# Kernel tuning notes

Measured on AMD Instinct MI355X. Metric: run time of the kernel, lower is better.

The kernel has to match this reference:

```python
import jax, jax.numpy as jnp
import numpy as np

N_EMBD = 1024
N_HEAD = 16
BLOCK_SIZE = 2048
NEG_INF = -1e10


def _rope_cache(head_dim, max_positions):
    # theta_i = 10000^{-2i/dim}, freqs[t, i] = t * theta_i
    theta = 1.0 / (10000.0 ** (jnp.arange(0, head_dim, 2, dtype=jnp.float32) / head_dim))
    freqs = jnp.arange(max_positions, dtype=jnp.float32)[:, None] * theta[None, :]
    return jnp.cos(freqs), jnp.sin(freqs)  # each (max_positions, head_dim//2)


def _apply_rope(x, cos, sin):
    # x: (B, nh, T, hs) interpreted as interleaved complex pairs
    B, nh, T, hs = x.shape
    xr = x.reshape(B, nh, T, hs // 2, 2)
    x0, x1 = xr[..., 0], xr[..., 1]
    c = cos[:T][None, None, :, :]
    s = sin[:T][None, None, :, :]
    o0 = x0 * c - x1 * s
    o1 = x0 * s + x1 * c
    return jnp.stack([o0, o1], axis=-1).reshape(B, nh, T, hs)


def setup_inputs() -> dict:
    key = jax.random.key(0)
    ks = jax.random.split(key, 9)
    B, T, C = 2, 2048, N_EMBD
    sc = 1.0 / np.sqrt(C)
    return {
        "x": jax.random.normal(ks[0], (B, T, C), jnp.float32),
        "Wq": jax.random.normal(ks[1], (C, C), jnp.float32) * sc,
        "bq": jax.random.normal(ks[2], (C,), jnp.float32) * 0.02,
        "Wk": jax.random.normal(ks[3], (C, C), jnp.float32) * sc,
        "bk": jax.random.normal(ks[4], (C,), jnp.float32) * 0.02,
        "Wv": jax.random.normal(ks[5], (C, C), jnp.float32) * sc,
        "bv": jax.random.normal(ks[6], (C,), jnp.float32) * 0.02,
        "Wp": jax.random.normal(ks[7], (C, C), jnp.float32) * sc,
        "bp": jax.random.normal(ks[8], (C,), jnp.float32) * 0.02,
    }


def reference(x, Wq, bq, Wk, bk, Wv, bv, Wp, bp):
    B, T, C = x.shape
    nh, hs = N_HEAD, C // N_HEAD

    def heads(W, b):
        return (x @ W.T + b).reshape(B, T, nh, hs).transpose(0, 2, 1, 3)

    q = heads(Wq, bq)
    k = heads(Wk, bk)
    v = heads(Wv, bv)

    cos, sin = _rope_cache(hs, BLOCK_SIZE)
    q = _apply_rope(q, cos, sin)
    k = _apply_rope(k, cos, sin)

    att = jnp.einsum("bhqd,bhkd->bhqk", q, k) * (1.0 / np.sqrt(hs))
    causal = jnp.tril(jnp.ones((T, T), dtype=bool))
    att = jnp.where(causal[None, None], att, NEG_INF)
    att = jax.nn.softmax(att, axis=-1)
    y = jnp.einsum("bhqk,bhkd->bhqd", att, v)
    y = y.transpose(0, 2, 1, 3).reshape(B, T, C)
    return y @ Wp.T + bp
```

## Files before the change

### kernel.cpp

```cpp
#include <hip/hip_runtime.h>

typedef __bf16 bf16;
typedef short  s16;
typedef s16   s16x8 __attribute__((ext_vector_type(8)));
typedef bf16  bf16x4 __attribute__((ext_vector_type(4)));
typedef float f32x4 __attribute__((ext_vector_type(4)));

#define B_SZ 2
#define T_SEQ 2048
#define C_DIM 1024
#define NH 16
#define HS 64
#define M_TOT (B_SZ * T_SEQ)

#define NEG_BIG (-30000.0f)
#define LOG2_10000 13.287712379549449f
#define Q_PRESCALE 0.18033688011112042f


__device__ __forceinline__ float san(float x) {
    unsigned u = __float_as_uint(x);
    return ((u & 0x7F800000u) == 0x7F800000u) ? 0.f : x;
}

__device__ __forceinline__ void load16_lds(const bf16* g, void* lds_base) {
    __builtin_amdgcn_global_load_lds(
        (const __attribute__((address_space(1))) void*)g,
        (__attribute__((address_space(3))) void*)lds_base, 16, 0, 0);
}

#define CVT_GRID 8448

__global__ __launch_bounds__(256) void cvt_bf16_kernel(
    const float* __restrict__ x,  const float* __restrict__ wq,
    const float* __restrict__ wk, const float* __restrict__ wv,
    const float* __restrict__ wp,
    bf16* __restrict__ xb, bf16* __restrict__ wqb, bf16* __restrict__ wkb,
    bf16* __restrict__ wvb, bf16* __restrict__ wpb,
    float* __restrict__ cs, float* __restrict__ sn)
{
    const int b = blockIdx.x;
    if (b >= 8192) {
        const int idx = (b - 8192) * 256 + threadIdx.x;
        const int t = idx >> 5, i = idx & 31;
        const float theta = __builtin_exp2f(-(float)(2 * i) * (LOG2_10000 / 64.f));
        const float a = (float)t * theta;
        cs[idx] = san(cosf(a));
        sn[idx] = san(sinf(a));
        return;
    }
    int z, base;
    if (b < 4096) { z = 0; base = b; }
    else          { z = 1 + ((b - 4096) >> 10); base = (b - 4096) & 1023; }

    const float* src = (z == 0) ? x : (z == 1) ? wq : (z == 2) ? wk : (z == 3) ? wv : wp;
    bf16* dst = (z == 0) ? xb : (z == 1) ? wqb : (z == 2) ? wkb : (z == 3) ? wvb : wpb;

    const int i = (base * 256 + threadIdx.x) * 4;
    const float4 v = *(const float4*)(src + i);
    bf16x4 o;
    o[0] = (bf16)v.x; o[1] = (bf16)v.y; o[2] = (bf16)v.z; o[3] = (bf16)v.w;
    *(bf16x4*)(dst + i) = o;
}

#define QSTAGE(bufi, kk)                                                       \
    load16_lds(gA + (kk),               (char*)(sA[bufi]) + w * 1024);         \
    load16_lds(gA + 128 * C_DIM + (kk), (char*)(sA[bufi]) + 8192 + w * 1024);  \
    load16_lds(gB + (kk),               (char*)(sB[bufi]) + w * 1024);         \
    load16_lds(gB + 128 * C_DIM + (kk), (char*)(sB[bufi]) + 8192 + w * 1024);

__global__ __launch_bounds__(512, 2) void qkv_gemm(
    const bf16* __restrict__ X, const bf16* __restrict__ W_all,
    const float* __restrict__ bq, const float* __restrict__ bk,
    const float* __restrict__ bv,
    const float* __restrict__ cs_tab, const float* __restrict__ sn_tab,
    bf16* __restrict__ q_ws, bf16* __restrict__ k_ws, bf16* __restrict__ vt_ws)
{
    __shared__ __attribute__((aligned(16))) bf16 sA[3][256 * 32];
    __shared__ __attribute__((aligned(16))) bf16 sB[3][256 * 32];

    const int m0 = blockIdx.x * 256;
    const int n0 = blockIdx.y * 256;
    const int mode = blockIdx.y >> 2;

    const int t = threadIdx.x;
    const int w = t >> 6;
    const int lane = t & 63;
    const int qd = lane >> 4;
    const int r  = lane & 15;
    const int qs = qd ^ ((r >> 1) & 3);
    const int wm = w >> 2, wn = w & 3;
    const int srow = t >> 2;
    const int scol = ((t & 3) ^ ((t >> 3) & 3)) * 8;
    const bf16* gA = X + (size_t)(m0 + srow) * C_DIM + scol;
    const bf16* gB = W_all + (size_t)(n0 + srow) * C_DIM + scol;

    f32x4 acc[8][4] = {};

    QSTAGE(0, 0)
    QSTAGE(1, 32)
    #pragma unroll
    for (int kt_ = 0; kt_ < 32; kt_++) {
        __builtin_amdgcn_sched_barrier(0);
        if (kt_ < 30) asm volatile("s_waitcnt vmcnt(4) lgkmcnt(0)" ::: "memory");
        else          asm volatile("s_waitcnt vmcnt(0) lgkmcnt(0)" ::: "memory");
        __builtin_amdgcn_sched_barrier(0);
        __builtin_amdgcn_s_barrier();
        __builtin_amdgcn_sched_barrier(0);
        if (kt_ + 2 < 32) { QSTAGE((kt_ + 2) % 3, (kt_ + 2) * 32) }
        {
            const bf16* pA = sA[kt_ % 3];
            const bf16* pB = sB[kt_ % 3];
            s16x8 af[8], bfr[4];
            #pragma unroll
            for (int mt = 0; mt < 8; mt++)
                af[mt] = *(const s16x8*)(pA + (wm * 128 + mt * 16 + r) * 32 + qs * 8);
            #pragma unroll
            for (int nt = 0; nt < 4; nt++)
                bfr[nt] = *(const s16x8*)(pB + (wn * 64 + nt * 16 + r) * 32 + qs * 8);
            #pragma unroll
            for (int mt = 0; mt < 8; mt++)
                #pragma unroll
                for (int nt = 0; nt < 4; nt++)
                    acc[mt][nt] = __builtin_amdgcn_mfma_f32_16x16x32_bf16(
                        af[mt], bfr[nt], acc[mt][nt], 0, 0, 0);
        }
    }

    const float* bias = (mode == 0) ? bq : (mode == 1) ? bk : bv;

    if (mode == 2) {
        #pragma unroll
        for (int mt = 0; mt < 8; mt++) {
            const int mrow0 = m0 + wm * 128 + mt * 16 + qd * 4;
            const int bb = mrow0 >> 11;
            const int t0 = mrow0 & 2047;
            #pragma unroll
            for (int nt = 0; nt < 4; nt++) {
                const int cm = (n0 & 1023) + wn * 64 + nt * 16 + r;
                const int h = cm >> 6, d = cm & 63;
                const float bv_ = bias[cm];
                bf16x4 pk;
                #pragma unroll
                for (int reg = 0; reg < 4; reg++)
                    pk[reg] = (bf16)san(acc[mt][nt][reg] + bv_);
                *(bf16x4*)(vt_ws + ((size_t)(bb * NH + h) * HS + d) * T_SEQ + t0) = pk;
            }
        }
    } else {
        bf16* out = (mode == 0) ? q_ws : k_ws;
        const float post = (mode == 0) ? Q_PRESCALE : 1.0f;
        #pragma unroll
        for (int mt = 0; mt < 8; mt++) {
            const int mrow0 = m0 + wm * 128 + mt * 16 + qd * 4;
            const int bb = mrow0 >> 11;
            const int t0 = mrow0 & 2047;
            #pragma unroll
            for (int nt = 0; nt < 4; nt++) {
                const int cm = (n0 & 1023) + wn * 64 + nt * 16 + r;
                const int h = cm >> 6, d = cm & 63;
                const int pi = d >> 1;
                const float bv_ = bias[cm];
                #pragma unroll
                for (int reg = 0; reg < 4; reg++) {
                    const int tt = t0 + reg;
                    float v = san(acc[mt][nt][reg] + bv_);
                    float partner = __shfl_xor(v, 1);
                    float c = cs_tab[tt * 32 + pi];
                    float s = sn_tab[tt * 32 + pi];
                    float rot = (d & 1) ? (v * c + partner * s)
                                        : (v * c - partner * s);
                    out[((size_t)(bb * NH + h) * T_SEQ + tt) * HS + d] =
                        (bf16)san(rot * post);
                }
            }
        }
    }
}

#define STAGE3(bufi, kk)                                                       \
    load16_lds(gA0 + (kk), (char*)(sA + (bufi) * 2048) + w * 1024);            \
    load16_lds(gB0 + (kk), (char*)(sB + (bufi) * 4096) + w * 1024);            \
    load16_lds(gB1 + (kk), (char*)(sB + (bufi) * 4096) + 4096 + w * 1024);

#define K_STEP3(bufi)                                                          \
    {                                                                          \
        const bf16* pA = sA + (bufi) * 2048;                                   \
        const bf16* pB = sB + (bufi) * 4096;                                   \
        s16x8 af[2], bfr[4];                                                   \
        _Pragma("unroll")                                                      \
        for (int mt = 0; mt < 2; mt++)                                         \
            af[mt] = *(const s16x8*)(pA + (wm * 32 + mt * 16 + r) * 32 + qs * 8); \
        _Pragma("unroll")                                                      \
        for (int nt = 0; nt < 4; nt++)                                         \
            bfr[nt] = *(const s16x8*)(pB + (wn * 64 + nt * 16 + r) * 32 + qs * 8); \
        _Pragma("unroll")                                                      \
        for (int mt = 0; mt < 2; mt++)                                         \
            _Pragma("unroll")                                                  \
            for (int nt = 0; nt < 4; nt++)                                     \
                acc[mt][nt] = __builtin_amdgcn_mfma_f32_16x16x32_bf16(         \
                    af[mt], bfr[nt], acc[mt][nt], 0, 0, 0);                    \
    }

#define GEMM_CORE(Xp, Wp_)                                                     \
    const int t = threadIdx.x;                                                 \
    const int w = t >> 6;                                                      \
    const int lane = t & 63;                                                   \
    const int qd = lane >> 4;                                                  \
    const int r  = lane & 15;                                                  \
    const int qs = qd ^ ((r >> 1) & 3);                                        \
    const int wm = w & 1, wn = w >> 1;                                         \
    const int srow = t >> 2;                                                   \
    const int scol = ((t & 3) ^ ((t >> 3) & 3)) * 8;                           \
    const bf16* gA0 = (Xp) + (size_t)(m0 + srow) * C_DIM + scol;               \
    const bf16* gB0 = (Wp_) + (size_t)(n0 + srow) * C_DIM + scol;              \
    const bf16* gB1 = (Wp_) + (size_t)(n0 + 64 + srow) * C_DIM + scol;         \
    f32x4 acc[2][4] = {};                                                      \
    STAGE3(0, 0)                                                               \
    STAGE3(1, 32)                                                              \
    _Pragma("unroll")                                                          \
    for (int kt_ = 0; kt_ < 32; kt_++) {                                       \
        __builtin_amdgcn_sched_barrier(0);                                     \
        if (kt_ < 30) asm volatile("s_waitcnt vmcnt(3) lgkmcnt(0)" ::: "memory"); \
        else          asm volatile("s_waitcnt vmcnt(0) lgkmcnt(0)" ::: "memory"); \
        __builtin_amdgcn_sched_barrier(0);                                     \
        __builtin_amdgcn_s_barrier();                                          \
        __builtin_amdgcn_sched_barrier(0);                                     \
        if (kt_ + 2 < 32) { STAGE3((kt_ + 2) % 3, (kt_ + 2) * 32) }            \
        K_STEP3(kt_ % 3)                                                       \
    }

__global__ __launch_bounds__(256) void proj_gemm(
    const bf16* __restrict__ Y, const bf16* __restrict__ Wp,
    const float* __restrict__ bp, float* __restrict__ out)
{
    __shared__ __attribute__((aligned(16))) bf16 sA[3 * 64 * 32];
    __shared__ __attribute__((aligned(16))) bf16 sB[3 * 128 * 32];

    const int m0 = blockIdx.x * 64;
    const int n0 = blockIdx.y * 128;

    GEMM_CORE(Y, Wp)

    #pragma unroll
    for (int mt = 0; mt < 2; mt++) {
        const int mrow0 = m0 + wm * 32 + mt * 16 + qd * 4;
        #pragma unroll
        for (int nt = 0; nt < 4; nt++) {
            const int col = n0 + wn * 64 + nt * 16 + r;
            const float bv_ = bp[col];
            #pragma unroll
            for (int reg = 0; reg < 4; reg++)
                out[(size_t)(mrow0 + reg) * C_DIM + col] = san(acc[mt][nt][reg] + bv_);
        }
    }
}

__global__ __launch_bounds__(256) void attn_kernel(
    const bf16* __restrict__ q_ws, const bf16* __restrict__ k_ws,
    const bf16* __restrict__ vt_ws, bf16* __restrict__ y_ws)
{
    __shared__ __attribute__((aligned(16))) bf16 sK[2][2][64][32];
    __shared__ __attribute__((aligned(16))) bf16 sV[2][2][64][32];
    __shared__ __attribute__((aligned(16))) bf16 sP[4][16][72];

    const int id = (int)blockIdx.x;
    const int qt = 31 - (id >> 5);
    const int j  = id & 31;
    const int bh = (j & 7) + 8 * (j >> 3);

    const int w    = threadIdx.x >> 6;
    const int lane = threadIdx.x & 63;
    const int qd = lane >> 4;
    const int r  = lane & 15;
    const int qs = qd ^ ((r >> 1) & 3);
    const int ps = 4 * (r & 3);

    const bf16* Qb = q_ws + (size_t)bh * T_SEQ * HS;
    const bf16* Kb = k_ws + (size_t)bh * T_SEQ * HS;
    const bf16* Vb = vt_ws + (size_t)bh * HS * T_SEQ;

    const int srow = lane >> 2;
    const int scol = ((lane & 3) ^ ((lane >> 3) & 3)) * 8;
    const bf16* Kb_w = Kb + (size_t)(w * 16 + srow) * HS + scol;
    const bf16* Vb_w = Vb + (size_t)(w * 16 + srow) * T_SEQ + scol;

    bf16 (*pw)[72] = sP[w];
    const int bb = bh >> 4, h = bh & 15;

    const int q0 = qt * 64 + w * 16;

    s16x8 aq0 = *(const s16x8*)(Qb + (size_t)(q0 + r) * HS + qd * 8);
    s16x8 aq1 = *(const s16x8*)(Qb + (size_t)(q0 + r) * HS + 32 + qd * 8);

    f32x4 o[4] = {};
    float l_lane = 0.f;

    load16_lds(Kb_w,      &sK[0][0][w * 16][0]);
    load16_lds(Kb_w + 32, &sK[0][1][w * 16][0]);
    load16_lds(Vb_w,      &sV[0][0][w * 16][0]);
    load16_lds(Vb_w + 32, &sV[0][1][w * 16][0]);

    for (int kt = 0; kt <= qt; kt++) {
        const int cur = kt & 1;
        __syncthreads();

        if (kt < qt) {
            const bf16* kp = Kb_w + (size_t)(kt + 1) * 64 * HS;
            const bf16* vp = Vb_w + (kt + 1) * 64;
            load16_lds(kp,      &sK[cur ^ 1][0][w * 16][0]);
            load16_lds(kp + 32, &sK[cur ^ 1][1][w * 16][0]);
            load16_lds(vp,      &sV[cur ^ 1][0][w * 16][0]);
            load16_lds(vp + 32, &sV[cur ^ 1][1][w * 16][0]);
        }

        f32x4 s[4];
        __builtin_amdgcn_s_setprio(1);
        #pragma unroll
        for (int c = 0; c < 4; c++) {
            s16x8 k0 = *(const s16x8*)&sK[cur][0][c * 16 + r][qs * 8];
            s16x8 k1 = *(const s16x8*)&sK[cur][1][c * 16 + r][qs * 8];
            f32x4 z = {};
            z = __builtin_amdgcn_mfma_f32_16x16x32_bf16(k0, aq0, z, 0, 0, 0);
            z = __builtin_amdgcn_mfma_f32_16x16x32_bf16(k1, aq1, z, 0, 0, 0);
            s[c] = z;
        }
        __builtin_amdgcn_s_setprio(0);

        if (kt == qt) {
            const int qg = q0 + r;
            #pragma unroll
            for (int c = 0; c < 4; c++)
                #pragma unroll
                for (int reg = 0; reg < 4; reg++) {
                    const int kg = kt * 64 + c * 16 + qd * 4 + reg;
                    s[c][reg] = (kg <= qg) ? s[c][reg] : NEG_BIG;
                }
        }

        #pragma unroll
        for (int c = 0; c < 4; c++) {
            bf16x4 pk;
            #pragma unroll
            for (int reg = 0; reg < 4; reg++) {
                float p = __builtin_exp2f(s[c][reg]);
                l_lane += p;
                pk[reg] = (bf16)p;
            }
            *(bf16x4*)&pw[r][((4 * c + qd) ^ ps) * 4] = pk;
        }

        s16x8 ap0 = *(const s16x8*)&pw[r][((2 * qd) ^ ps) * 4];
        s16x8 ap1 = *(const s16x8*)&pw[r][((8 + 2 * qd) ^ ps) * 4];
        __builtin_amdgcn_s_setprio(1);
        #pragma unroll
        for (int nt = 0; nt < 4; nt++) {
            s16x8 av0 = *(const s16x8*)&sV[cur][0][nt * 16 + r][qs * 8];
            s16x8 av1 = *(const s16x8*)&sV[cur][1][nt * 16 + r][qs * 8];
            o[nt] = __builtin_amdgcn_mfma_f32_16x16x32_bf16(av0, ap0, o[nt], 0, 0, 0);
            o[nt] = __builtin_amdgcn_mfma_f32_16x16x32_bf16(av1, ap1, o[nt], 0, 0, 0);
        }
        __builtin_amdgcn_s_setprio(0);
    }

    float l = l_lane;
    l += __shfl_xor(l, 16);
    l += __shfl_xor(l, 32);
    const float inv = 1.f / fmaxf(l, 1e-20f);

    const int q = q0 + r;
    bf16* dst = y_ws + ((size_t)(bb * T_SEQ + q) * NH + h) * HS;
    #pragma unroll
    for (int nt = 0; nt < 4; nt++) {
        bf16x4 pk;
        #pragma unroll
        for (int reg = 0; reg < 4; reg++)
            pk[reg] = (bf16)san(o[nt][reg] * inv);
        *(bf16x4*)(dst + nt * 16 + qd * 4) = pk;
    }
}

extern "C" void kernel_launch(void* const* d_in, const int* in_sizes, int n_in,
                              void* d_out, int out_size, void* d_ws, size_t ws_size,
                              hipStream_t stream)
{
    const size_t MB = 1024 * 1024;
    const size_t NEED = 40 * MB + 2 * 65536 * sizeof(float);
    if (ws_size < NEED || n_in < 9) return;

    const float* x  = (const float*)d_in[0];
    const float* Wq = (const float*)d_in[1];
    const float* bq = (const float*)d_in[2];
    const float* Wk = (const float*)d_in[3];
    const float* bk = (const float*)d_in[4];
    const float* Wv = (const float*)d_in[5];
    const float* bv = (const float*)d_in[6];
    const float* Wp = (const float*)d_in[7];
    const float* bp = (const float*)d_in[8];
    float* out = (float*)d_out;

    char* ws = (char*)d_ws;
    bf16*  q_ws   = (bf16*)(ws + 0 * MB);
    bf16*  k_ws   = (bf16*)(ws + 8 * MB);
    bf16*  vt_ws  = (bf16*)(ws + 16 * MB);
    bf16*  x_b    = (bf16*)(ws + 24 * MB);
    bf16*  y_ws   = (bf16*)(ws + 24 * MB);
    bf16*  Wq_b   = (bf16*)(ws + 32 * MB);
    bf16*  Wk_b   = (bf16*)(ws + 34 * MB);
    bf16*  Wv_b   = (bf16*)(ws + 36 * MB);
    bf16*  Wp_b   = (bf16*)(ws + 38 * MB);
    float* cs_tab = (float*)(ws + 40 * MB);
    float* sn_tab = cs_tab + 65536;
    const bf16* W_all = Wq_b;

    cvt_bf16_kernel<<<dim3(CVT_GRID), 256, 0, stream>>>(
        x, Wq, Wk, Wv, Wp, x_b, Wq_b, Wk_b, Wv_b, Wp_b, cs_tab, sn_tab);
    qkv_gemm<<<dim3(M_TOT / 256, 3 * C_DIM / 256), 512, 0, stream>>>(
        x_b, W_all, bq, bk, bv, cs_tab, sn_tab, q_ws, k_ws, vt_ws);
    attn_kernel<<<dim3(32 * 32), 256, 0, stream>>>(
        q_ws, k_ws, vt_ws, y_ws);
    proj_gemm<<<dim3(M_TOT / 64, C_DIM / 128), 256, 0, stream>>>(
        y_ws, Wp_b, bp, out);
}
```

Baseline: 184.1 us.

## Process two adjacent query tiles per attention block to share K/V loads

Each attention workgroup now handles a pair of consecutive 64-row query tiles (qtB and qtA = qtB+1) for the same head, so every K/V tile loaded into LDS and the K fragments read from it are reused by both tiles. The grid halves to 512 blocks, and the last diagonal K tile is handled in a separate epilogue for the upper tile only. This cuts K/V global and LDS traffic per query row and evens out causal work per block. In exchange it uses more registers for the doubled Q, score and accumulator state, which may lower occupancy, and leaves fewer blocks to fill the GPU.

After: 215.7 us. 17.2% more time.

```diff
diff --git a/kernel.cpp b/kernel.cpp
--- a/kernel.cpp
+++ b/kernel.cpp
@@ -256,18 +256,50 @@
     }
 }
 
+
+#define ATT_QK(sv, aq0_, aq1_)                                                 \
+    _Pragma("unroll")                                                          \
+    for (int c = 0; c < 4; c++) {                                              \
+        f32x4 z = {};                                                          \
+        z = __builtin_amdgcn_mfma_f32_16x16x32_bf16(kf0[c], aq0_, z, 0, 0, 0); \
+        z = __builtin_amdgcn_mfma_f32_16x16x32_bf16(kf1[c], aq1_, z, 0, 0, 0); \
+        sv[c] = z;                                                             \
+    }
+
+#define ATT_MASK(sv, qg)                                                       \
+    _Pragma("unroll")                                                          \
+    for (int c = 0; c < 4; c++)                                                \
+        _Pragma("unroll")                                                      \
+        for (int reg = 0; reg < 4; reg++) {                                    \
+            const int kg = kt * 64 + c * 16 + qd * 4 + reg;                    \
+            sv[c][reg] = (kg <= (qg)) ? sv[c][reg] : NEG_BIG;                  \
+        }
+
+#define ATT_SM(sv, pbuf, lacc)                                                 \
+    _Pragma("unroll")                                                          \
+    for (int c = 0; c < 4; c++) {                                              \
+        bf16x4 pk;                                                             \
+        _Pragma("unroll")                                                      \
+        for (int reg = 0; reg < 4; reg++) {                                    \
+            float p = __builtin_exp2f(sv[c][reg]);                             \
+            lacc += p;                                                         \
+            pk[reg] = (bf16)p;                                                 \
+        }                                                                      \
+        *(bf16x4*)&pbuf[r][((4 * c + qd) ^ ps) * 4] = pk;                      \
+    }
+
 __global__ __launch_bounds__(256) void attn_kernel(
     const bf16* __restrict__ q_ws, const bf16* __restrict__ k_ws,
     const bf16* __restrict__ vt_ws, bf16* __restrict__ y_ws)
 {
     __shared__ __attribute__((aligned(16))) bf16 sK[2][2][64][32];
     __shared__ __attribute__((aligned(16))) bf16 sV[2][2][64][32];
-    __shared__ __attribute__((aligned(16))) bf16 sP[4][16][72];
+    __shared__ __attribute__((aligned(16))) bf16 sP[2][4][16][72];
 
     const int id = (int)blockIdx.x;
-    const int qt = 31 - (id >> 5);
-    const int j  = id & 31;
-    const int bh = (j & 7) + 8 * (j >> 3);
+    const int bh = (id & 7) + 8 * (id >> 7);
+    const int pr = 15 - ((id >> 3) & 15);
+    const int qtB = 2 * pr, qtA = qtB + 1;
 
     const int w    = threadIdx.x >> 6;
     const int lane = threadIdx.x & 63;
@@ -285,27 +317,31 @@
     const bf16* Kb_w = Kb + (size_t)(w * 16 + srow) * HS + scol;
     const bf16* Vb_w = Vb + (size_t)(w * 16 + srow) * T_SEQ + scol;
 
-    bf16 (*pw)[72] = sP[w];
+    bf16 (*pwA)[72] = sP[0][w];
+    bf16 (*pwB)[72] = sP[1][w];
     const int bb = bh >> 4, h = bh & 15;
 
-    const int q0 = qt * 64 + w * 16;
-
-    s16x8 aq0 = *(const s16x8*)(Qb + (size_t)(q0 + r) * HS + qd * 8);
-    s16x8 aq1 = *(const s16x8*)(Qb + (size_t)(q0 + r) * HS + 32 + qd * 8);
-
-    f32x4 o[4] = {};
-    float l_lane = 0.f;
+    const int q0A = qtA * 64 + w * 16;
+    const int q0B = qtB * 64 + w * 16;
+
+    s16x8 aqA0 = *(const s16x8*)(Qb + (size_t)(q0A + r) * HS + qd * 8);
+    s16x8 aqA1 = *(const s16x8*)(Qb + (size_t)(q0A + r) * HS + 32 + qd * 8);
+    s16x8 aqB0 = *(const s16x8*)(Qb + (size_t)(q0B + r) * HS + qd * 8);
+    s16x8 aqB1 = *(const s16x8*)(Qb + (size_t)(q0B + r) * HS + 32 + qd * 8);
+
+    f32x4 oA[4] = {}, oB[4] = {};
+    float lA = 0.f, lB = 0.f;
 
     load16_lds(Kb_w,      &sK[0][0][w * 16][0]);
     load16_lds(Kb_w + 32, &sK[0][1][w * 16][0]);
     load16_lds(Vb_w,      &sV[0][0][w * 16][0]);
     load16_lds(Vb_w + 32, &sV[0][1][w * 16][0]);
 
-    for (int kt = 0; kt <= qt; kt++) {
+    for (int kt = 0; kt <= qtB; kt++) {
         const int cur = kt & 1;
         __syncthreads();
 
-        if (kt < qt) {
+        {
             const bf16* kp = Kb_w + (size_t)(kt + 1) * 64 * HS;
             const bf16* vp = Vb_w + (kt + 1) * 64;
             load16_lds(kp,      &sK[cur ^ 1][0][w * 16][0]);
@@ -314,69 +350,100 @@
             load16_lds(vp + 32, &sV[cur ^ 1][1][w * 16][0]);
         }
 
-        f32x4 s[4];
+        s16x8 kf0[4], kf1[4];
+        #pragma unroll
+        for (int c = 0; c < 4; c++) {
+            kf0[c] = *(const s16x8*)&sK[cur][0][c * 16 + r][qs * 8];
+            kf1[c] = *(const s16x8*)&sK[cur][1][c * 16 + r][qs * 8];
+        }
+        f32x4 sa[4], sb[4];
         __builtin_amdgcn_s_setprio(1);
-        #pragma unroll
-        for (int c = 0; c < 4; c++) {
-            s16x8 k0 = *(const s16x8*)&sK[cur][0][c * 16 + r][qs * 8];
-            s16x8 k1 = *(const s16x8*)&sK[cur][1][c * 16 + r][qs * 8];
-            f32x4 z = {};
-            z = __builtin_amdgcn_mfma_f32_16x16x32_bf16(k0, aq0, z, 0, 0, 0);
-            z = __builtin_amdgcn_mfma_f32_16x16x32_bf16(k1, aq1, z, 0, 0, 0);
-            s[c] = z;
-        }
+        ATT_QK(sa, aqA0, aqA1)
+        ATT_QK(sb, aqB0, aqB1)
         __builtin_amdgcn_s_setprio(0);
 
-        if (kt == qt) {
-            const int qg = q0 + r;
-            #pragma unroll
-            for (int c = 0; c < 4; c++)
-                #pragma unroll
-                for (int reg = 0; reg < 4; reg++) {
-                    const int kg = kt * 64 + c * 16 + qd * 4 + reg;
-                    s[c][reg] = (kg <= qg) ? s[c][reg] : NEG_BIG;
-                }
-        }
-
-        #pragma unroll
-        for (int c = 0; c < 4; c++) {
-            bf16x4 pk;
-            #pragma unroll
-            for (int reg = 0; reg < 4; reg++) {
-                float p = __builtin_exp2f(s[c][reg]);
-                l_lane += p;
-                pk[reg] = (bf16)p;
-            }
-            *(bf16x4*)&pw[r][((4 * c + qd) ^ ps) * 4] = pk;
-        }
-
-        s16x8 ap0 = *(const s16x8*)&pw[r][((2 * qd) ^ ps) * 4];
-        s16x8 ap1 = *(const s16x8*)&pw[r][((8 + 2 * qd) ^ ps) * 4];
+        if (kt == qtB) { ATT_MASK(sb, q0B + r) }
+
+        ATT_SM(sa, pwA, lA)
+        ATT_SM(sb, pwB, lB)
+
+        s16x8 apA0 = *(const s16x8*)&pwA[r][((2 * qd) ^ ps) * 4];
+        s16x8 apA1 = *(const s16x8*)&pwA[r][((8 + 2 * qd) ^ ps) * 4];
+        s16x8 apB0 = *(const s16x8*)&pwB[r][((2 * qd) ^ ps) * 4];
+        s16x8 apB1 = *(const s16x8*)&pwB[r][((8 + 2 * qd) ^ ps) * 4];
         __builtin_amdgcn_s_setprio(1);
         #pragma unroll
         for (int nt = 0; nt < 4; nt++) {
             s16x8 av0 = *(const s16x8*)&sV[cur][0][nt * 16 + r][qs * 8];
             s16x8 av1 = *(const s16x8*)&sV[cur][1][nt * 16 + r][qs * 8];
-            o[nt] = __builtin_amdgcn_mfma_f32_16x16x32_bf16(av0, ap0, o[nt], 0, 0, 0);
-            o[nt] = __builtin_amdgcn_mfma_f32_16x16x32_bf16(av1, ap1, o[nt], 0, 0, 0);
+            oA[nt] = __builtin_amdgcn_mfma_f32_16x16x32_bf16(av0, apA0, oA[nt], 0, 0, 0);
+            oA[nt] = __builtin_amdgcn_mfma_f32_16x16x32_bf16(av1, apA1, oA[nt], 0, 0, 0);
+            oB[nt] = __builtin_amdgcn_mfma_f32_16x16x32_bf16(av0, apB0, oB[nt], 0, 0, 0);
+            oB[nt] = __builtin_amdgcn_mfma_f32_16x16x32_bf16(av1, apB1, oB[nt], 0, 0, 0);
         }
         __builtin_amdgcn_s_setprio(0);
     }
 
-    float l = l_lane;
-    l += __shfl_xor(l, 16);
-    l += __shfl_xor(l, 32);
-    const float inv = 1.f / fmaxf(l, 1e-20f);
-
-    const int q = q0 + r;
-    bf16* dst = y_ws + ((size_t)(bb * T_SEQ + q) * NH + h) * HS;
-    #pragma unroll
-    for (int nt = 0; nt < 4; nt++) {
-        bf16x4 pk;
-        #pragma unroll
-        for (int reg = 0; reg < 4; reg++)
-            pk[reg] = (bf16)san(o[nt][reg] * inv);
-        *(bf16x4*)(dst + nt * 16 + qd * 4) = pk;
+    {
+        const int kt = qtA;
+        const int cur = kt & 1;
+        __syncthreads();
+
+        s16x8 kf0[4], kf1[4];
+        #pragma unroll
+        for (int c = 0; c < 4; c++) {
+            kf0[c] = *(const s16x8*)&sK[cur][0][c * 16 + r][qs * 8];
+            kf1[c] = *(const s16x8*)&sK[cur][1][c * 16 + r][qs * 8];
+        }
+        f32x4 sa[4];
+        __builtin_amdgcn_s_setprio(1);
+        ATT_QK(sa, aqA0, aqA1)
+        __builtin_amdgcn_s_setprio(0);
+        ATT_MASK(sa, q0A + r)
+        ATT_SM(sa, pwA, lA)
+
+        s16x8 apA0 = *(const s16x8*)&pwA[r][((2 * qd) ^ ps) * 4];
+        s16x8 apA1 = *(const s16x8*)&pwA[r][((8 + 2 * qd) ^ ps) * 4];
+        __builtin_amdgcn_s_setprio(1);
+        #pragma unroll
+        for (int nt = 0; nt < 4; nt++) {
+            s16x8 av0 = *(const s16x8*)&sV[cur][0][nt * 16 + r][qs * 8];
+            s16x8 av1 = *(const s16x8*)&sV[cur][1][nt * 16 + r][qs * 8];
+            oA[nt] = __builtin_amdgcn_mfma_f32_16x16x32_bf16(av0, apA0, oA[nt], 0, 0, 0);
+            oA[nt] = __builtin_amdgcn_mfma_f32_16x16x32_bf16(av1, apA1, oA[nt], 0, 0, 0);
+        }
+        __builtin_amdgcn_s_setprio(0);
+    }
+
+    {
+        float l = lA;
+        l += __shfl_xor(l, 16);
+        l += __shfl_xor(l, 32);
+        const float inv = 1.f / fmaxf(l, 1e-20f);
+        bf16* dst = y_ws + ((size_t)(bb * T_SEQ + q0A + r) * NH + h) * HS;
+        #pragma unroll
+        for (int nt = 0; nt < 4; nt++) {
+            bf16x4 pk;
+            #pragma unroll
+            for (int reg = 0; reg < 4; reg++)
+                pk[reg] = (bf16)san(oA[nt][reg] * inv);
+            *(bf16x4*)(dst + nt * 16 + qd * 4) = pk;
+        }
+    }
+    {
+        float l = lB;
+        l += __shfl_xor(l, 16);
+        l += __shfl_xor(l, 32);
+        const float inv = 1.f / fmaxf(l, 1e-20f);
+        bf16* dst = y_ws + ((size_t)(bb * T_SEQ + q0B + r) * NH + h) * HS;
+        #pragma unroll
+        for (int nt = 0; nt < 4; nt++) {
+            bf16x4 pk;
+            #pragma unroll
+            for (int reg = 0; reg < 4; reg++)
+                pk[reg] = (bf16)san(oB[nt][reg] * inv);
+            *(bf16x4*)(dst + nt * 16 + qd * 4) = pk;
+        }
     }
 }
 
@@ -417,7 +484,7 @@
         x, Wq, Wk, Wv, Wp, x_b, Wq_b, Wk_b, Wv_b, Wp_b, cs_tab, sn_tab);
     qkv_gemm<<<dim3(M_TOT / 256, 3 * C_DIM / 256), 512, 0, stream>>>(
         x_b, W_all, bq, bk, bv, cs_tab, sn_tab, q_ws, k_ws, vt_ws);
-    attn_kernel<<<dim3(32 * 32), 256, 0, stream>>>(
+    attn_kernel<<<dim3(512), 256, 0, stream>>>(
         q_ws, k_ws, vt_ws, y_ws);
     proj_gemm<<<dim3(M_TOT / 64, C_DIM / 128), 256, 0, stream>>>(
         y_ws, Wp_b, bp, out);
```
